# Performance work log

Measured on AMD Instinct MI355X. Metric: run time of the kernel, lower is better.

The kernel has to match this reference:

```python
import jax, jax.numpy as jnp
import numpy as np


def setup_inputs() -> dict:
    key = jax.random.key(0)
    k1, k2 = jax.random.split(key)
    N_NODES, MAX_DEGREE, BATCH = 100000, 128, 262144
    # adj_info: padded adjacency lists, entries are node ids in [0, N_NODES)
    adj_info = jax.random.randint(k1, (N_NODES, MAX_DEGREE), 0, N_NODES, dtype=jnp.int32)
    ids = jax.random.randint(k2, (BATCH,), 0, N_NODES, dtype=jnp.int32)
    return {"adj_info": adj_info, "ids": ids, "num_samples": 25}


def reference(adj_info, ids, num_samples):
    # embedding_lookup: gather adjacency rows -> [B, max_degree]
    adj_lists = jnp.take(adj_info, ids, axis=0)
    # weights are a copy of the adjacency entries in the original module
    # tf.random_shuffle on the transposed [D, B] tensor permutes the neighbor
    # axis with a SINGLE permutation shared across all rows.
    max_degree = adj_lists.shape[1]
    perm = jax.random.permutation(jax.random.key(42), max_degree)
    shuffled = adj_lists[:, perm]                  # [B, max_degree]
    adj_sampled = shuffled[:, :num_samples]        # slice first num_samples
    weights_sampled = shuffled[:, :num_samples]
    return adj_sampled, weights_sampled
```

## Files before the change

### kernel.cpp

```cpp
#include <hip/hip_runtime.h>
#include <algorithm>
#include <cstdint>


static inline void threefry2x32_block(uint32_t k0, uint32_t k1,
                                      uint32_t& x0, uint32_t& x1) {
  auto rotl = [](uint32_t v, int d) { return (v << d) | (v >> (32 - d)); };
  const int r0[4] = {13, 15, 26, 6};
  const int r1[4] = {17, 29, 16, 24};
  const uint32_t ks0 = k0, ks1 = k1, ks2 = k0 ^ k1 ^ 0x1BD11BDAu;
  x0 += ks0; x1 += ks1;
  for (int i = 0; i < 4; ++i) { x0 += x1; x1 = rotl(x1, r0[i]); x1 ^= x0; }
  x0 += ks1; x1 += ks2 + 1u;
  for (int i = 0; i < 4; ++i) { x0 += x1; x1 = rotl(x1, r1[i]); x1 ^= x0; }
  x0 += ks2; x1 += ks0 + 2u;
  for (int i = 0; i < 4; ++i) { x0 += x1; x1 = rotl(x1, r0[i]); x1 ^= x0; }
  x0 += ks0; x1 += ks1 + 3u;
  for (int i = 0; i < 4; ++i) { x0 += x1; x1 = rotl(x1, r1[i]); x1 ^= x0; }
  x0 += ks1; x1 += ks2 + 4u;
  for (int i = 0; i < 4; ++i) { x0 += x1; x1 = rotl(x1, r0[i]); x1 ^= x0; }
  x0 += ks2; x1 += ks0 + 5u;
}

struct Perm25 { int p[25]; };

static Perm25 compute_perm25() {
  uint32_t sk0 = 0u, sk1 = 1u;
  threefry2x32_block(0u, 42u, sk0, sk1);

  uint32_t bits[128];
  for (int i = 0; i < 128; ++i) {
    uint32_t x0 = 0u, x1 = (uint32_t)i;
    threefry2x32_block(sk0, sk1, x0, x1);
    bits[i] = x0 ^ x1;
  }

  int idxs[128];
  for (int i = 0; i < 128; ++i) idxs[i] = i;
  std::stable_sort(idxs, idxs + 128,
                   [&](int a, int b) { return bits[a] < bits[b]; });

  Perm25 out;
  for (int j = 0; j < 25; ++j) out.p[j] = idxs[j];
  return out;
}


#define NS 25
#define MAX_DEG 128

__global__ __launch_bounds__(256)
void uniform_sampler_kernel(const int* __restrict__ adj,
                            const int* __restrict__ ids,
                            int* __restrict__ out,
                            Perm25 perm, int batch) {
  const int idx = blockIdx.x * blockDim.x + threadIdx.x;
  const int total = batch * NS;
  if (idx >= total) return;
  const unsigned b = (unsigned)idx / NS;
  const int j = idx - (int)b * NS;
  const int node = ids[b];
  const int v = adj[(size_t)node * MAX_DEG + perm.p[j]];
  out[idx] = v;
  out[total + idx] = v;
}

extern "C" void kernel_launch(void* const* d_in, const int* in_sizes, int n_in,
                              void* d_out, int out_size, void* d_ws, size_t ws_size,
                              hipStream_t stream) {
  const int* adj = (const int*)d_in[0];
  const int* ids = (const int*)d_in[1];

  const int batch = in_sizes[1];
  const int total = batch * NS;

  const Perm25 perm = compute_perm25();

  const int block = 256;
  const int grid = (total + block - 1) / block;
  uniform_sampler_kernel<<<grid, block, 0, stream>>>(adj, ids, (int*)d_out,
                                                     perm, batch);
}
```

Measured before the change: 33.39 us.

## Stage full adjacency rows in LDS and emit vectorized permuted output

Each block cooperatively loads 32 full adjacency rows into shared memory with 16-byte loads, then selects the 25 permuted columns from LDS and writes output with int4 stores. This replaces scattered 4-byte global gathers and scalar stores with coalesced vector transactions. It reads the whole 128-entry row instead of only the sampled entries, increasing bytes fetched, and adds two block barriers.

```diff
diff --git a/kernel.cpp b/kernel.cpp
--- a/kernel.cpp
+++ b/kernel.cpp
@@ -48,21 +48,57 @@
 
 #define NS 25
 #define MAX_DEG 128
+#define ROWS_PER_BLOCK 32
+#define LDS_STRIDE 132
+#define ELEMS (ROWS_PER_BLOCK * NS)
 
 __global__ __launch_bounds__(256)
 void uniform_sampler_kernel(const int* __restrict__ adj,
                             const int* __restrict__ ids,
                             int* __restrict__ out,
                             Perm25 perm, int batch) {
-  const int idx = blockIdx.x * blockDim.x + threadIdx.x;
-  const int total = batch * NS;
-  if (idx >= total) return;
-  const unsigned b = (unsigned)idx / NS;
-  const int j = idx - (int)b * NS;
-  const int node = ids[b];
-  const int v = adj[(size_t)node * MAX_DEG + perm.p[j]];
-  out[idx] = v;
-  out[total + idx] = v;
+  __shared__ int s_rows[ROWS_PER_BLOCK * LDS_STRIDE];
+  __shared__ int s_ids[ROWS_PER_BLOCK];
+  __shared__ int s_perm[NS];
+
+  const int tid = threadIdx.x;
+  const int row0 = blockIdx.x * ROWS_PER_BLOCK;
+
+  if (tid < ROWS_PER_BLOCK) {
+    const int gr = row0 + tid;
+    s_ids[tid] = (gr < batch) ? ids[gr] : 0;
+  }
+  if (tid < NS) s_perm[tid] = perm.p[tid];
+  __syncthreads();
+
+#pragma unroll
+  for (int it = 0; it < 4; ++it) {
+    const int r = it * 8 + (tid >> 5);
+    const int c = tid & 31;
+    const int node = s_ids[r];
+    const int4 v =
+        *reinterpret_cast<const int4*>(adj + (size_t)node * MAX_DEG + c * 4);
+    *reinterpret_cast<int4*>(&s_rows[r * LDS_STRIDE + c * 4]) = v;
+  }
+  __syncthreads();
+
+  if (tid < ELEMS / 4) {
+    int vals[4];
+#pragma unroll
+    for (int e = 0; e < 4; ++e) {
+      const int li = tid * 4 + e;
+      const unsigned r = (unsigned)li / NS;
+      const int j = li - (int)r * NS;
+      vals[e] = s_rows[r * LDS_STRIDE + s_perm[j]];
+    }
+    const int4 v = make_int4(vals[0], vals[1], vals[2], vals[3]);
+    const size_t base = (size_t)blockIdx.x * ELEMS + (size_t)tid * 4;
+    const size_t total = (size_t)batch * NS;
+    if (base + 4 <= total) {
+      *reinterpret_cast<int4*>(out + base) = v;
+      *reinterpret_cast<int4*>(out + total + base) = v;
+    }
+  }
 }
 
 extern "C" void kernel_launch(void* const* d_in, const int* in_sizes, int n_in,
@@ -72,12 +108,10 @@
   const int* ids = (const int*)d_in[1];
 
   const int batch = in_sizes[1];
-  const int total = batch * NS;
 
   const Perm25 perm = compute_perm25();
 
-  const int block = 256;
-  const int grid = (total + block - 1) / block;
-  uniform_sampler_kernel<<<grid, block, 0, stream>>>(adj, ids, (int*)d_out,
-                                                     perm, batch);
+  const int grid = (batch + ROWS_PER_BLOCK - 1) / ROWS_PER_BLOCK;
+  uniform_sampler_kernel<<<grid, 256, 0, stream>>>(adj, ids, (int*)d_out,
+                                                   perm, batch);
 }
```

Measured after the change: 32.08 us. 1.04x faster.
